# Kernel optimization log

Measured on AMD Instinct MI355X. Metric: run time of the kernel, lower is better.

The kernel has to match this reference:

```python
import jax, jax.numpy as jnp
import numpy as np

D = 1024
ITERATIONS = 2


def setup_inputs() -> dict:
    key = jax.random.key(0)
    ks = jax.random.split(key, 7)
    s = 1.0 / np.sqrt(D)  # PyTorch GRUCell/Linear init scale
    x = jax.random.normal(ks[0], (8, 4096, D), dtype=jnp.float32)
    W_ih = jax.random.uniform(ks[1], (3 * D, D), minval=-s, maxval=s, dtype=jnp.float32)
    W_hh = jax.random.uniform(ks[2], (3 * D, D), minval=-s, maxval=s, dtype=jnp.float32)
    b_ih = jax.random.uniform(ks[3], (3 * D,), minval=-s, maxval=s, dtype=jnp.float32)
    b_hh = jax.random.uniform(ks[4], (3 * D,), minval=-s, maxval=s, dtype=jnp.float32)
    We = jax.random.uniform(ks[5], (1, D), minval=-s, maxval=s, dtype=jnp.float32)
    be = jax.random.uniform(ks[6], (1,), minval=-s, maxval=s, dtype=jnp.float32)
    return {"x": x, "W_ih": W_ih, "W_hh": W_hh, "b_ih": b_ih, "b_hh": b_hh, "We": We, "be": be}


def _gru_cell(inp, h, W_ih, W_hh, b_ih, b_hh):
    # PyTorch GRUCell gate order: r, z, n
    gi = inp @ W_ih.T + b_ih  # [N, 3D]
    gh = h @ W_hh.T + b_hh    # [N, 3D]
    i_r, i_z, i_n = jnp.split(gi, 3, axis=-1)
    h_r, h_z, h_n = jnp.split(gh, 3, axis=-1)
    r = jax.nn.sigmoid(i_r + h_r)
    z = jax.nn.sigmoid(i_z + h_z)
    n = jnp.tanh(i_n + r * h_n)
    return (1.0 - z) * n + z * h


def reference(x, W_ih, W_hh, b_ih, b_hh, We, be):
    B, S, Dm = x.shape
    state = x.reshape(-1, Dm)  # [B*S, D]
    for _ in range(ITERATIONS):
        error = jax.nn.sigmoid(state @ We.T + be)  # [B*S, 1]
        new_state = _gru_cell(state, state, W_ih, W_hh, b_ih, b_hh)
        state = (1.0 - error) * state + error * new_state
    return state.reshape(B, S, Dm)
```

## Files before the change

### kernel.cpp

```cpp
#include <hip/hip_runtime.h>

#define DD 1024

typedef int   i32x4  __attribute__((ext_vector_type(4)));
typedef int   i32x8  __attribute__((ext_vector_type(8)));
typedef float f32x4  __attribute__((ext_vector_type(4)));

__device__ __forceinline__ float sigm(float x) { return 1.0f / (1.0f + __expf(-x)); }
__device__ __forceinline__ float tanh_fast(float x) {
  float e = __expf(-2.0f * fabsf(x));
  float t = (1.0f - e) / (1.0f + e);
  return copysignf(t, x);
}
__device__ __forceinline__ void gload_lds16(const void* g, void* l) {
  __builtin_amdgcn_global_load_lds((const __attribute__((address_space(1))) void*)g,
                                   (__attribute__((address_space(3))) void*)l, 16, 0, 0);
}
__device__ __forceinline__ unsigned pk_fp8x4(float a, float b, float c, float d) {
  int u = __builtin_amdgcn_cvt_pk_fp8_f32(a, b, 0, false);
  u = __builtin_amdgcn_cvt_pk_fp8_f32(c, d, u, true);
  return (unsigned)u;
}


__global__ __launch_bounds__(256) void prep_weights(
    const float* __restrict__ Wih, const float* __restrict__ Whh,
    const float* __restrict__ bih, const float* __restrict__ bhh,
    unsigned char* __restrict__ Wcat8, float* __restrict__ bias) {
  int i = blockIdx.x * 256 + threadIdx.x;
  int g = i >> 18;
  int rem = i & 262143;
  int n = rem >> 8;
  int k4 = rem & 255;
  const float4* wih4 = reinterpret_cast<const float4*>(Wih);
  const float4* whh4 = reinterpret_cast<const float4*>(Whh);
  float4 v;
  if (g == 0) {
    size_t idx = (size_t)n * 256 + k4;
    float4 a = wih4[idx], b = whh4[idx];
    v = make_float4(a.x + b.x, a.y + b.y, a.z + b.z, a.w + b.w);
  } else if (g == 1) {
    size_t idx = (size_t)(DD + n) * 256 + k4;
    float4 a = wih4[idx], b = whh4[idx];
    v = make_float4(a.x + b.x, a.y + b.y, a.z + b.z, a.w + b.w);
  } else if (g == 2) {
    size_t idx = (size_t)(2 * DD + n) * 256 + k4;
    v = wih4[idx];
  } else {
    size_t idx = (size_t)(2 * DD + n) * 256 + k4;
    v = whh4[idx];
  }
  unsigned pkd = pk_fp8x4(v.x * 32.0f, v.y * 32.0f, v.z * 32.0f, v.w * 32.0f);

  int db  = n >> 5;
  int dgl = n & 31;
  int n_t = (dgl >> 4) * 64 + g * 16 + (dgl & 15);
  int kt   = k4 >> 5;
  int gran = (k4 >> 2) & 7;
  int klo  = (k4 & 3) * 4;
  size_t addr = (size_t)db * 131072 + kt * 16384 + (n_t >> 3) * 1024 +
                gran * 128 + (n_t & 7) * 16 + klo;
  *reinterpret_cast<unsigned*>(Wcat8 + addr) = pkd;

  if (i < 4 * DD) {
    int bg = i >> 10, bn = i & 1023;
    float bv;
    if (bg == 0)      bv = bih[bn] + bhh[bn];
    else if (bg == 1) bv = bih[DD + bn] + bhh[DD + bn];
    else if (bg == 2) bv = bih[2 * DD + bn];
    else              bv = bhh[2 * DD + bn];
    bias[i] = bv;
  }
}

__global__ __launch_bounds__(256) void error_cast(
    const float* S, const float* __restrict__ We, const float* __restrict__ be,
    unsigned char* __restrict__ Sb8, float* __restrict__ err) {
  __shared__ float part[4];
  const int row = blockIdx.x;
  const int t = threadIdx.x;
  float4 v = reinterpret_cast<const float4*>(S + (size_t)row * DD)[t];
  float4 w = reinterpret_cast<const float4*>(We)[t];
  float dot = v.x * w.x + v.y * w.y + v.z * w.z + v.w * w.w;

  int kt   = t >> 5;
  int gran = (t >> 2) & 7;
  int klo  = (t & 3) * 4;
  int r    = row & 127;
  size_t addr = (size_t)(row >> 7) * 131072 + kt * 16384 + (r >> 3) * 1024 +
                gran * 128 + (r & 7) * 16 + klo;
  *reinterpret_cast<unsigned*>(Sb8 + addr) = pk_fp8x4(v.x, v.y, v.z, v.w);

#pragma unroll
  for (int off = 32; off > 0; off >>= 1) dot += __shfl_xor(dot, off);
  if ((t & 63) == 0) part[t >> 6] = dot;
  __syncthreads();
  if (t == 0) err[row] = sigm(part[0] + part[1] + part[2] + part[3] + be[0]);
}

__global__ __launch_bounds__(256, 2) void gru_fused_gemm(
    const unsigned char* __restrict__ Sb8,
    const unsigned char* __restrict__ Wcat8,
    const float* __restrict__ bias,
    const float* __restrict__ err,
    const float* Sf,
    float* out, int M) {
  __shared__ alignas(16) unsigned char As[2 * 16384];
  __shared__ alignas(16) unsigned char Bs[2 * 16384];

  const int bid = blockIdx.x;
  const int x = bid & 7;
  const int c = bid >> 3;
  const int db = (x & 1) * 16 + (c & 15);
  const int rb = (x >> 1) * 64 + (c >> 4);

  const int tid = threadIdx.x;
  const int w = tid >> 6;
  const int lane = tid & 63;
  const int l15 = lane & 15;
  const int q = lane >> 4;
  const int wr = w >> 1, wc = w & 1;

  const unsigned char* srcA0 = Sb8 + (size_t)rb * 131072 + lane * 16;
  const unsigned char* srcB0 = Wcat8 + (size_t)db * 131072 + lane * 16;

  const int abase = (wr * 8 + (l15 >> 3)) * 1024 + 2 * q * 128 + (l15 & 7) * 16;
  const int bbase = (wc * 8 + (l15 >> 3)) * 1024 + 2 * q * 128 + (l15 & 7) * 16;

  f32x4 acc[4][4];
#pragma unroll
  for (int mi = 0; mi < 4; ++mi)
#pragma unroll
    for (int g = 0; g < 4; ++g) acc[mi][g] = f32x4{0.f, 0.f, 0.f, 0.f};

  auto stage = [&](int t) {
    const int slot = (t & 1) * 16384;
    const int koff = t * 16384;
#pragma unroll
    for (int i = 0; i < 4; ++i) {
      const int j = (w + i * 4) * 1024;
      gload_lds16(srcA0 + koff + j, As + j + slot);
      gload_lds16(srcB0 + koff + j, Bs + j + slot);
    }
  };

  stage(0);
  stage(1);

  for (int t = 0; t < 8; ++t) {
    const int sb = (t & 1) * 16384;
    if (t < 7) asm volatile("s_waitcnt vmcnt(8)" ::: "memory");
    else       asm volatile("s_waitcnt vmcnt(0)" ::: "memory");
    __builtin_amdgcn_s_barrier();

    const unsigned char* Ab = As + sb;
    const unsigned char* Bb = Bs + sb;
    i32x8 a[4], b[4];
#pragma unroll
    for (int mi = 0; mi < 4; ++mi) {
      i32x4 a0 = *reinterpret_cast<const i32x4*>(Ab + abase + mi * 2048);
      i32x4 a1 = *reinterpret_cast<const i32x4*>(Ab + abase + mi * 2048 + 128);
      a[mi] = __builtin_shufflevector(a0, a1, 0, 1, 2, 3, 4, 5, 6, 7);
    }
#pragma unroll
    for (int g = 0; g < 4; ++g) {
      i32x4 b0 = *reinterpret_cast<const i32x4*>(Bb + bbase + g * 2048);
      i32x4 b1 = *reinterpret_cast<const i32x4*>(Bb + bbase + g * 2048 + 128);
      b[g] = __builtin_shufflevector(b0, b1, 0, 1, 2, 3, 4, 5, 6, 7);
    }
    asm volatile("s_waitcnt lgkmcnt(0)" ::: "memory");
    __builtin_amdgcn_s_barrier();

    if (t <= 5) stage(t + 2);

    __builtin_amdgcn_s_setprio(1);
#pragma unroll
    for (int g = 0; g < 4; ++g)
#pragma unroll
      for (int mi = 0; mi < 4; ++mi)
        acc[mi][g] = __builtin_amdgcn_mfma_scale_f32_16x16x128_f8f6f4(
            a[mi], b[g], acc[mi][g], 0, 0, 0, 0x7F7F7F7F, 0, 0x7A7A7A7A);
    __builtin_amdgcn_s_setprio(0);
  }

  const int dgcol = db * 32 + wc * 16 + l15;
  const float b_r = bias[dgcol];
  const float b_z = bias[DD + dgcol];
  const float b_i = bias[2 * DD + dgcol];
  const float b_h = bias[3 * DD + dgcol];
#pragma unroll
  for (int mi = 0; mi < 4; ++mi) {
#pragma unroll
    for (int j = 0; j < 4; ++j) {
      int m = rb * 128 + wr * 64 + mi * 16 + q * 4 + j;
      float e = err[m];
      float hh = Sf[(size_t)m * DD + dgcol];
      float r = sigm(acc[mi][0][j] + b_r);
      float z = sigm(acc[mi][1][j] + b_z);
      float n = tanh_fast(acc[mi][2][j] + b_i + r * (acc[mi][3][j] + b_h));
      out[(size_t)m * DD + dgcol] = hh + e * (1.0f - z) * (n - hh);
    }
  }
}

extern "C" void kernel_launch(void* const* d_in, const int* in_sizes, int n_in,
                              void* d_out, int out_size, void* d_ws, size_t ws_size,
                              hipStream_t stream) {
  const float* x   = (const float*)d_in[0];
  const float* Wih = (const float*)d_in[1];
  const float* Whh = (const float*)d_in[2];
  const float* bih = (const float*)d_in[3];
  const float* bhh = (const float*)d_in[4];
  const float* We  = (const float*)d_in[5];
  const float* be  = (const float*)d_in[6];
  float* out = (float*)d_out;
  const int M = in_sizes[0] / DD;

  char* ws = (char*)d_ws;
  unsigned char* Sb8   = (unsigned char*)ws;
  unsigned char* Wcat8 = (unsigned char*)(ws + (size_t)M * DD);
  float* bias = (float*)(ws + (size_t)M * DD + (size_t)4 * DD * DD);
  float* err  = (float*)(ws + (size_t)M * DD + (size_t)4 * DD * DD + (size_t)4 * DD * 4);

  prep_weights<<<4096, 256, 0, stream>>>(Wih, Whh, bih, bhh, Wcat8, bias);

  const int nwg = (M / 128) * 32;
  const float* S = x;
  for (int it = 0; it < 2; ++it) {
    error_cast<<<M, 256, 0, stream>>>(S, We, be, Sb8, err);
    gru_fused_gemm<<<nwg, 256, 0, stream>>>(Sb8, Wcat8, bias, err, S, out, M);
    S = out;
  }
}
```

Before: 525.3 us.

## Load GEMM fragments directly from global into registers, dropping LDS staging

Replaces the double-buffered global-to-LDS staging and barriers with direct global loads of MFMA fragments into a register double buffer, prefetching the next K tile while computing the current one. This removes LDS traffic and workgroup barriers, but each wave now loads its own A/B fragments, so pairs of waves load the same data again from global/L2. Register pressure also rises, which may hurt occupancy under the two-blocks-per-CU launch bound.

```diff
diff --git a/kernel.cpp b/kernel.cpp
--- a/kernel.cpp
+++ b/kernel.cpp
@@ -11,10 +11,6 @@
   float e = __expf(-2.0f * fabsf(x));
   float t = (1.0f - e) / (1.0f + e);
   return copysignf(t, x);
-}
-__device__ __forceinline__ void gload_lds16(const void* g, void* l) {
-  __builtin_amdgcn_global_load_lds((const __attribute__((address_space(1))) void*)g,
-                                   (__attribute__((address_space(3))) void*)l, 16, 0, 0);
 }
 __device__ __forceinline__ unsigned pk_fp8x4(float a, float b, float c, float d) {
   int u = __builtin_amdgcn_cvt_pk_fp8_f32(a, b, 0, false);
@@ -105,9 +101,6 @@
     const float* __restrict__ err,
     const float* Sf,
     float* out, int M) {
-  __shared__ alignas(16) unsigned char As[2 * 16384];
-  __shared__ alignas(16) unsigned char Bs[2 * 16384];
-
   const int bid = blockIdx.x;
   const int x = bid & 7;
   const int c = bid >> 3;
@@ -121,11 +114,9 @@
   const int q = lane >> 4;
   const int wr = w >> 1, wc = w & 1;
 
-  const unsigned char* srcA0 = Sb8 + (size_t)rb * 131072 + lane * 16;
-  const unsigned char* srcB0 = Wcat8 + (size_t)db * 131072 + lane * 16;
-
-  const int abase = (wr * 8 + (l15 >> 3)) * 1024 + 2 * q * 128 + (l15 & 7) * 16;
-  const int bbase = (wc * 8 + (l15 >> 3)) * 1024 + 2 * q * 128 + (l15 & 7) * 16;
+  const int lanoff = (l15 >> 3) * 1024 + 2 * q * 128 + (l15 & 7) * 16;
+  const unsigned char* Ab = Sb8 + (size_t)rb * 131072 + wr * 8192 + lanoff;
+  const unsigned char* Bb = Wcat8 + (size_t)db * 131072 + wc * 8192 + lanoff;
 
   f32x4 acc[4][4];
 #pragma unroll
@@ -133,55 +124,43 @@
 #pragma unroll
     for (int g = 0; g < 4; ++g) acc[mi][g] = f32x4{0.f, 0.f, 0.f, 0.f};
 
-  auto stage = [&](int t) {
-    const int slot = (t & 1) * 16384;
-    const int koff = t * 16384;
-#pragma unroll
-    for (int i = 0; i < 4; ++i) {
-      const int j = (w + i * 4) * 1024;
-      gload_lds16(srcA0 + koff + j, As + j + slot);
-      gload_lds16(srcB0 + koff + j, Bs + j + slot);
+  i32x8 abuf[2][4], bbuf[2][4];
+
+#define LOAD_TILE(T, BUFI)                                                     \
+  {                                                                            \
+    const unsigned char* Abt = Ab + (T) * 16384;                               \
+    const unsigned char* Bbt = Bb + (T) * 16384;                               \
+    _Pragma("unroll")                                                          \
+    for (int mi = 0; mi < 4; ++mi) {                                           \
+      i32x4 lo = *reinterpret_cast<const i32x4*>(Abt + mi * 2048);             \
+      i32x4 hi = *reinterpret_cast<const i32x4*>(Abt + mi * 2048 + 128);       \
+      abuf[BUFI][mi] = __builtin_shufflevector(lo, hi, 0, 1, 2, 3, 4, 5, 6, 7);\
+    }                                                                          \
+    _Pragma("unroll")                                                          \
+    for (int g = 0; g < 4; ++g) {                                              \
+      i32x4 lo = *reinterpret_cast<const i32x4*>(Bbt + g * 2048);              \
+      i32x4 hi = *reinterpret_cast<const i32x4*>(Bbt + g * 2048 + 128);        \
+      bbuf[BUFI][g] = __builtin_shufflevector(lo, hi, 0, 1, 2, 3, 4, 5, 6, 7); \
+    }                                                                          \
+  }
+
+  LOAD_TILE(0, 0)
+#pragma unroll
+  for (int t = 0; t < 8; ++t) {
+    if (t < 7) {
+      if ((t & 1) == 0) LOAD_TILE(t + 1, 1)
+      else              LOAD_TILE(t + 1, 0)
     }
-  };
-
-  stage(0);
-  stage(1);
-
-  for (int t = 0; t < 8; ++t) {
-    const int sb = (t & 1) * 16384;
-    if (t < 7) asm volatile("s_waitcnt vmcnt(8)" ::: "memory");
-    else       asm volatile("s_waitcnt vmcnt(0)" ::: "memory");
-    __builtin_amdgcn_s_barrier();
-
-    const unsigned char* Ab = As + sb;
-    const unsigned char* Bb = Bs + sb;
-    i32x8 a[4], b[4];
-#pragma unroll
-    for (int mi = 0; mi < 4; ++mi) {
-      i32x4 a0 = *reinterpret_cast<const i32x4*>(Ab + abase + mi * 2048);
-      i32x4 a1 = *reinterpret_cast<const i32x4*>(Ab + abase + mi * 2048 + 128);
-      a[mi] = __builtin_shufflevector(a0, a1, 0, 1, 2, 3, 4, 5, 6, 7);
-    }
-#pragma unroll
-    for (int g = 0; g < 4; ++g) {
-      i32x4 b0 = *reinterpret_cast<const i32x4*>(Bb + bbase + g * 2048);
-      i32x4 b1 = *reinterpret_cast<const i32x4*>(Bb + bbase + g * 2048 + 128);
-      b[g] = __builtin_shufflevector(b0, b1, 0, 1, 2, 3, 4, 5, 6, 7);
-    }
-    asm volatile("s_waitcnt lgkmcnt(0)" ::: "memory");
-    __builtin_amdgcn_s_barrier();
-
-    if (t <= 5) stage(t + 2);
-
-    __builtin_amdgcn_s_setprio(1);
+    const int cur = t & 1;
 #pragma unroll
     for (int g = 0; g < 4; ++g)
 #pragma unroll
       for (int mi = 0; mi < 4; ++mi)
         acc[mi][g] = __builtin_amdgcn_mfma_scale_f32_16x16x128_f8f6f4(
-            a[mi], b[g], acc[mi][g], 0, 0, 0, 0x7F7F7F7F, 0, 0x7A7A7A7A);
-    __builtin_amdgcn_s_setprio(0);
-  }
+            abuf[cur][mi], bbuf[cur][g], acc[mi][g], 0, 0, 0,
+            0x7F7F7F7F, 0, 0x7A7A7A7A);
+  }
+#undef LOAD_TILE
 
   const int dgcol = db * 32 + wc * 16 + l15;
   const float b_r = bias[dgcol];
```

Result: slower. 549.4 us (+4.6%).
